# Kernel optimization log

Hardware: AMD Instinct MI355X
Metric: run time of the kernel (lower is better)

The kernel has to match this reference:

```python
import jax, jax.numpy as jnp
import numpy as np

B, S, N, H, F, L, Lt = 2, 8, 150, 128, 40, 2, 1
EF = 2 * F + 2  # 82: src feat + dst feat + distance + bond
_rows_np, _cols_np = np.where(~np.eye(N, dtype=bool))  # fully connected, no self loops
_rows = jnp.asarray(_rows_np)
_cols = jnp.asarray(_cols_np)
E = _rows_np.shape[0]


def setup_inputs() -> dict:
    key = jax.random.key(0)
    ks = jax.random.split(key, 20)
    w = lambda k, shape: 0.1 * jax.random.normal(k, shape, dtype=jnp.float32)
    d = {}
    d['t'] = jax.random.uniform(ks[0], (B, 1), dtype=jnp.float32)
    d['x'] = jax.random.normal(ks[1], (B, S, N, 3), dtype=jnp.float32)
    d['peptide_seq'] = jax.random.randint(ks[2], (B, 15), 0, 20)
    d['atom_labels'] = jax.random.randint(ks[3], (B, N), 0, 5)
    d['amino_acid_pos'] = jax.random.randint(ks[4], (B, N), 1, 16)
    d['bond_matrix'] = (jax.random.uniform(ks[5], (B, N, N)) < 0.1).astype(jnp.float32)
    d['edge_mask'] = jnp.ones((B, N, N), jnp.float32)
    d['atom_mask'] = jnp.ones((B, N, 1), jnp.float32)
    d['restore_indices'] = jnp.tile(jnp.eye(N, dtype=jnp.float32)[None], (B, 1, 1))
    d['W_e1'] = w(ks[6], (L, EF, H)); d['b_e1'] = jnp.zeros((L, H), jnp.float32)
    d['W_e2'] = w(ks[7], (L, H, H)); d['b_e2'] = jnp.zeros((L, H), jnp.float32)
    d['W_c'] = w(ks[8], (L, H, 1)); d['b_c'] = jnp.zeros((L, 1), jnp.float32)
    d['W_h'] = w(ks[9], (L, F + H, F)); d['b_h'] = jnp.zeros((L, F), jnp.float32)
    d['w_t'] = w(ks[10], (L, 1, H)); d['w_b_t'] = jnp.zeros((L, H), jnp.float32)
    d['tW_e1'] = w(ks[11], (Lt, EF, H)); d['tb_e1'] = jnp.zeros((Lt, H), jnp.float32)
    d['tW_e2'] = w(ks[12], (Lt, H, H)); d['tb_e2'] = jnp.zeros((Lt, H), jnp.float32)
    d['tW_c'] = w(ks[13], (Lt, H, 1)); d['tb_c'] = jnp.zeros((Lt, 1), jnp.float32)
    d['tW_h'] = w(ks[14], (Lt, F + H, F)); d['tb_h'] = jnp.zeros((Lt, F), jnp.float32)
    return d


def _forward(t, x, peptide_seq, atom_labels, amino_acid_pos, bond_matrix, edge_mask,
             atom_mask, restore_indices, W_e1, b_e1, W_e2, b_e2, W_c, b_c, W_h, b_h,
             w_t, w_b_t, tW_e1, tb_e1, tW_e2, tb_e2, tW_c, tb_c, tW_h, tb_h):
    # single-atom embedding: [B, N, 40]
    aa = jnp.take_along_axis(peptide_seq, amino_acid_pos - 1, axis=1)
    emb = jnp.concatenate([
        jax.nn.one_hot(atom_labels, 5, dtype=x.dtype),
        jax.nn.one_hot(aa, 20, dtype=x.dtype),
        jax.nn.one_hot(amino_acid_pos - 1, 15, dtype=x.dtype)], axis=-1)
    h = jnp.broadcast_to(emb[:, None], (B, S, N, F))
    # restore absolute coordinates: x[b,s,i,d] = sum_j x[b,s,j,d] * R[b,i,j]
    x = jnp.einsum('bsjd,bij->bsid', x, restore_indices)
    x0 = x
    # per-edge masks/features (gathered once; identical math to full cdist + indexing)
    em_e = edge_mask.reshape(B, 1, N * N)[:, :, _rows * N + _cols][..., None]  # [B,1,E,1]
    bond_e = jnp.broadcast_to(bond_matrix[:, _rows, _cols][:, None, :, None], (B, S, E, 1))

    def layer(x, h, We1, be1, We2, be2, Wc, bc, Wh, bh, temb):
        diff = x[:, :, _rows] - x[:, :, _cols]                      # [B,S,E,3]
        dist = jnp.sqrt(jnp.sum(diff * diff, -1, keepdims=True) + 1e-12)
        ef = jnp.concatenate([h[:, :, _rows], h[:, :, _cols], dist, bond_e], -1)  # [B,S,E,82]
        m = jax.nn.silu(ef @ We1 + be1 + temb)
        m = jax.nn.silu(m @ We2 + be2) * em_e                        # [B,S,E,H]
        cw = m @ Wc + bc                                             # [B,S,E,1]
        x_out = jnp.zeros_like(x).at[:, :, _rows].add(diff * cw) / (N - 1)
        agg = jnp.zeros((B, S, N, m.shape[-1]), m.dtype).at[:, :, _rows].add(m)
        h_out = jax.nn.silu(jnp.concatenate([h, agg], -1) @ Wh + bh)
        return x_out, h_out

    for l in range(L):
        temb = (t @ w_t[l] + w_b_t[l])[:, None, None, :]             # [B,1,1,H]
        xo, h = layer(x, h, W_e1[l], b_e1[l], W_e2[l], b_e2[l], W_c[l], b_c[l], W_h[l], b_h[l], temb)
        x = x + xo
    for l in range(Lt):
        xo, h = layer(x, h, tW_e1[l], tb_e1[l], tW_e2[l], tb_e2[l], tW_c[l], tb_c[l], tW_h[l], tb_h[l], 0.0)
        x = x + xo
    return (x - x0) * atom_mask[:, None, :, :]


def reference(t, x, peptide_seq, atom_labels, amino_acid_pos, bond_matrix, edge_mask,
              atom_mask, restore_indices, W_e1, b_e1, W_e2, b_e2, W_c, b_c, W_h, b_h,
              w_t, w_b_t, tW_e1, tb_e1, tW_e2, tb_e2, tW_c, tb_c, tW_h, tb_h):
    return _forward(t, x, peptide_seq, atom_labels, amino_acid_pos, bond_matrix, edge_mask,
                    atom_mask, restore_indices, W_e1, b_e1, W_e2, b_e2, W_c, b_c, W_h, b_h,
                    w_t, w_b_t, tW_e1, tb_e1, tW_e2, tb_e2, tW_c, tb_c, tW_h, tb_h)
```

## Files before the change

kernel.cpp:

```cpp
#include <hip/hip_runtime.h>
#include <math.h>

#define B_ 2
#define S_ 8
#define N_ 150
#define H_ 128
#define F_ 40
#define EF_ 82
#define NP_ 160
#define MPQ 136

typedef __attribute__((ext_vector_type(8))) short short8;
typedef __attribute__((ext_vector_type(4))) float float4v;

__device__ __forceinline__ float silu_f(float v) {
    return v * __builtin_amdgcn_rcpf(1.0f + __expf(-v));
}

__device__ __forceinline__ unsigned short f2bf(float f) {
    unsigned u = __builtin_bit_cast(unsigned, f);
    return (unsigned short)((u + 0x7fffu + ((u >> 16) & 1u)) >> 16);
}

__global__ void pack_we2_kernel(const float* __restrict__ w0,
                                const float* __restrict__ w1,
                                const float* __restrict__ w2,
                                unsigned short* __restrict__ outp) {
    int e = blockIdx.x * blockDim.x + threadIdx.x;
    int l = e >> 14, idx = e & 16383;
    int k = idx >> 7, c = idx & 127;
    const float* src = (l == 0) ? w0 : (l == 1) ? w1 : w2;
    outp[l * 16384 + c * H_ + k] = f2bf(src[idx]);
}

__global__ void restore_x_kernel(const float* __restrict__ x,
                                 const float* __restrict__ R,
                                 float* __restrict__ xa,
                                 float* __restrict__ x0) {
    int idx = blockIdx.x * blockDim.x + threadIdx.x;
    if (idx >= B_ * S_ * N_ * 3) return;
    int d = idx % 3;
    int i = (idx / 3) % N_;
    int bs = idx / (3 * N_);
    int b = bs / S_;
    const float* xrow = x + bs * N_ * 3 + d;
    const float* Rrow = R + (b * N_ + i) * N_;
    float acc = 0.0f;
    for (int j = 0; j < N_; j++) acc += xrow[j * 3] * Rrow[j];
    xa[idx] = acc;
    x0[idx] = acc;
}

__global__ void node0_kernel(const int* __restrict__ pep,
                             const int* __restrict__ labels,
                             const int* __restrict__ aapos,
                             const float* __restrict__ We1,
                             const float* __restrict__ be1,
                             const float* __restrict__ tp,
                             const float* __restrict__ wt,
                             const float* __restrict__ wbt,
                             float* __restrict__ h0,
                             float* __restrict__ Af,
                             float* __restrict__ Bf) {
    int bi = blockIdx.x;
    int b = bi / N_, i = bi % N_;
    int c = threadIdx.x;
    int al = labels[bi];
    int ap = aapos[bi];
    int aa = pep[b * 15 + ap - 1];
    int r0 = al, r1 = 5 + aa, r2 = 25 + ap - 1;
    float fa = We1[r0 * H_ + c] + We1[r1 * H_ + c] + We1[r2 * H_ + c]
             + be1[c] + tp[b] * wt[c] + wbt[c];
    float fb = We1[(F_ + r0) * H_ + c] + We1[(F_ + r1) * H_ + c] + We1[(F_ + r2) * H_ + c];
    float hv = 0.0f;
    if (c < F_) hv = (c == r0 || c == r1 || c == r2) ? 1.0f : 0.0f;
    for (int s = 0; s < S_; s++) {
        int n = (b * S_ + s) * N_ + i;
        Af[n * H_ + c] = fa;
        Bf[n * H_ + c] = fb;
        if (c < F_) h0[n * F_ + c] = hv;
    }
}

__global__ void node_kernel(const float* __restrict__ h_in,
                            const float* __restrict__ agg,
                            const float* __restrict__ Wh,
                            const float* __restrict__ bh,
                            const float* __restrict__ We1n,
                            const float* __restrict__ be1n,
                            const float* __restrict__ tp,
                            const float* __restrict__ wtn,
                            const float* __restrict__ wbtn,
                            int has_t,
                            float* __restrict__ h_out,
                            float* __restrict__ Af,
                            float* __restrict__ Bf) {
    int n = blockIdx.x;
    int b = n / (S_ * N_);
    int tid = threadIdx.x;
    __shared__ float cat[F_ + H_];
    __shared__ float part[120];
    __shared__ float hnew[F_];
    if (tid < F_) cat[tid] = h_in[n * F_ + tid];
    cat[F_ + tid] = agg[n * H_ + tid];
    __syncthreads();
    if (tid < 120) {
        int f = tid % 40, ks = tid / 40;
        float p = 0.0f;
        int k0 = ks * 56;
#pragma unroll 8
        for (int k = k0; k < k0 + 56; k++) p += cat[k] * Wh[k * F_ + f];
        part[tid] = p;
    }
    __syncthreads();
    if (tid < F_) {
        float hv = silu_f(part[tid] + part[40 + tid] + part[80 + tid] + bh[tid]);
        hnew[tid] = hv;
        h_out[n * F_ + tid] = hv;
    }
    __syncthreads();
    float fa = be1n[tid] + (has_t ? tp[b] * wtn[tid] + wbtn[tid] : 0.0f);
    float fb = 0.0f;
#pragma unroll 8
    for (int k = 0; k < F_; k++) {
        float hv = hnew[k];
        fa += hv * We1n[k * H_ + tid];
        fb += hv * We1n[(F_ + k) * H_ + tid];
    }
    Af[n * H_ + tid] = fa;
    Bf[n * H_ + tid] = fb;
}

__global__ __launch_bounds__(256, 4) void edge_kernel(
    const float* __restrict__ x_in,
    const float* __restrict__ Afeat,
    const float* __restrict__ Bfeat,
    const float* __restrict__ We1,
    const unsigned short* __restrict__ we2t,
    const float* __restrict__ be2,
    const float* __restrict__ Wc,
    const float* __restrict__ bcp,
    const float* __restrict__ bond,
    const float* __restrict__ emask,
    const float* __restrict__ x0v,
    const float* __restrict__ amask,
    int final_mode,
    float* __restrict__ x_out,
    float* __restrict__ agg_out)
{
    __shared__ __align__(16) short mbuf[2][16 * MPQ];
    __shared__ float4 diffE[NP_];
    __shared__ float2 dbL[NP_];
    __shared__ float DsumL[3];
    __shared__ float wpart[4][3];

    int blk = blockIdx.x;
    int i = blk % N_, bs = blk / N_, b = bs / S_;
    int tid = threadIdx.x;
    int node = bs * N_ + i;
    int lane = tid & 63, w = tid >> 6;
    int qd = lane >> 4, l15 = lane & 15;
    int rowLoc = tid >> 4, c0 = (tid & 15) * 8;

    float xi0 = x_in[node * 3 + 0];
    float xi1 = x_in[node * 3 + 1];
    float xi2 = x_in[node * 3 + 2];

    if (tid < NP_) {
        int j = tid;
        float xj0 = xi0, xj1 = xi1, xj2 = xi2, bnd = 0.0f, emv = 0.0f;
        if (j < N_) {
            int nj = bs * N_ + j;
            xj0 = x_in[nj * 3 + 0];
            xj1 = x_in[nj * 3 + 1];
            xj2 = x_in[nj * 3 + 2];
            int eij = (b * N_ + i) * N_ + j;
            bnd = bond[eij];
            emv = (j == i) ? 0.0f : emask[eij];
        }
        float d0 = xi0 - xj0, d1 = xi1 - xj1, d2 = xi2 - xj2;
        diffE[j] = make_float4(d0, d1, d2, emv);
        dbL[j] = make_float2(sqrtf(d0 * d0 + d1 * d1 + d2 * d2 + 1e-12f), bnd);
    }

    float afr[8], w80r[8], w81r[8];
    {
        float4 t0 = *(const float4*)&Afeat[node * H_ + c0];
        float4 t1 = *(const float4*)&Afeat[node * H_ + c0 + 4];
        afr[0]=t0.x; afr[1]=t0.y; afr[2]=t0.z; afr[3]=t0.w;
        afr[4]=t1.x; afr[5]=t1.y; afr[6]=t1.z; afr[7]=t1.w;
        t0 = *(const float4*)&We1[80 * H_ + c0];
        t1 = *(const float4*)&We1[80 * H_ + c0 + 4];
        w80r[0]=t0.x; w80r[1]=t0.y; w80r[2]=t0.z; w80r[3]=t0.w;
        w80r[4]=t1.x; w80r[5]=t1.y; w80r[6]=t1.z; w80r[7]=t1.w;
        t0 = *(const float4*)&We1[81 * H_ + c0];
        t1 = *(const float4*)&We1[81 * H_ + c0 + 4];
        w81r[0]=t0.x; w81r[1]=t0.y; w81r[2]=t0.z; w81r[3]=t0.w;
        w81r[4]=t1.x; w81r[5]=t1.y; w81r[6]=t1.z; w81r[7]=t1.w;
    }

    int ctb = w * 2;
    float b2r0 = be2[ctb * 16 + l15],  b2r1 = be2[ctb * 16 + 16 + l15];
    float wc0  = Wc[ctb * 16 + l15],   wc1  = Wc[ctb * 16 + 16 + l15];
    const unsigned short* bb0 = we2t + (ctb * 16 + l15) * H_ + qd * 8;
    const unsigned short* bb1 = bb0 + 16 * H_;
    short8 bf00 = *(const short8*)(bb0 +  0);
    short8 bf01 = *(const short8*)(bb0 + 32);
    short8 bf02 = *(const short8*)(bb0 + 64);
    short8 bf03 = *(const short8*)(bb0 + 96);
    short8 bf10 = *(const short8*)(bb1 +  0);
    short8 bf11 = *(const short8*)(bb1 + 32);
    short8 bf12 = *(const short8*)(bb1 + 64);
    short8 bf13 = *(const short8*)(bb1 + 96);

    __syncthreads();

    if (w == 0) {
        float p0 = 0, p1 = 0, p2 = 0;
        for (int j = lane; j < NP_; j += 64) {
            float4 d = diffE[j];
            p0 += d.x; p1 += d.y; p2 += d.z;
        }
        for (int s = 1; s < 64; s <<= 1) {
            p0 += __shfl_xor(p0, s, 64);
            p1 += __shfl_xor(p1, s, 64);
            p2 += __shfl_xor(p2, s, 64);
        }
        if (lane == 0) { DsumL[0] = p0; DsumL[1] = p1; DsumL[2] = p2; }
    }

    float aggP0 = 0, aggP1 = 0;
    float SP00 = 0, SP01 = 0, SP02 = 0, SP10 = 0, SP11 = 0, SP12 = 0;

    for (int jt = 0; jt < 10; jt++) {
        short* mb = mbuf[jt & 1];
        int jrow = jt * 16 + rowLoc;
        float mv[8];
        if (jrow < N_) {
            const float* bp = &Bfeat[(bs * N_ + jrow) * H_ + c0];
            float4 b0 = *(const float4*)bp;
            float4 b1 = *(const float4*)(bp + 4);
            float br[8] = {b0.x, b0.y, b0.z, b0.w, b1.x, b1.y, b1.z, b1.w};
            float2 db = dbL[jrow];
#pragma unroll
            for (int u = 0; u < 8; u++)
                mv[u] = silu_f(afr[u] + br[u] + db.x * w80r[u] + db.y * w81r[u]);
        } else {
#pragma unroll
            for (int u = 0; u < 8; u++) mv[u] = 0.0f;
        }
        short8 pkv;
#pragma unroll
        for (int u = 0; u < 8; u++) pkv[u] = (short)f2bf(mv[u]);
        *(short8*)&mb[rowLoc * MPQ + c0] = pkv;
        __syncthreads();

        const short* arow = &mb[l15 * MPQ + qd * 8];
        short8 a0 = *(const short8*)(arow +  0);
        short8 a1 = *(const short8*)(arow + 32);
        short8 a2 = *(const short8*)(arow + 64);
        short8 a3 = *(const short8*)(arow + 96);
        float4v acc0 = {0, 0, 0, 0}, acc1 = {0, 0, 0, 0};
        acc0 = __builtin_amdgcn_mfma_f32_16x16x32_bf16(a0, bf00, acc0, 0, 0, 0);
        acc1 = __builtin_amdgcn_mfma_f32_16x16x32_bf16(a0, bf10, acc1, 0, 0, 0);
        acc0 = __builtin_amdgcn_mfma_f32_16x16x32_bf16(a1, bf01, acc0, 0, 0, 0);
        acc1 = __builtin_amdgcn_mfma_f32_16x16x32_bf16(a1, bf11, acc1, 0, 0, 0);
        acc0 = __builtin_amdgcn_mfma_f32_16x16x32_bf16(a2, bf02, acc0, 0, 0, 0);
        acc1 = __builtin_amdgcn_mfma_f32_16x16x32_bf16(a2, bf12, acc1, 0, 0, 0);
        acc0 = __builtin_amdgcn_mfma_f32_16x16x32_bf16(a3, bf03, acc0, 0, 0, 0);
        acc1 = __builtin_amdgcn_mfma_f32_16x16x32_bf16(a3, bf13, acc1, 0, 0, 0);

#pragma unroll
        for (int r = 0; r < 4; r++) {
            int j = jt * 16 + qd * 4 + r;
            float4 de = diffE[j];
            float mv0 = silu_f(acc0[r] + b2r0) * de.w;
            float mv1 = silu_f(acc1[r] + b2r1) * de.w;
            aggP0 += mv0; aggP1 += mv1;
            SP00 += de.x * mv0; SP01 += de.y * mv0; SP02 += de.z * mv0;
            SP10 += de.x * mv1; SP11 += de.y * mv1; SP12 += de.z * mv1;
        }
    }

#define QR_(v) { v += __shfl_xor(v, 16, 64); v += __shfl_xor(v, 32, 64); }
    QR_(aggP0) QR_(aggP1)
    QR_(SP00) QR_(SP01) QR_(SP02)
    QR_(SP10) QR_(SP11) QR_(SP12)
#undef QR_

    if (!final_mode && qd == 0) {
        agg_out[node * H_ + ctb * 16 + l15]      = aggP0;
        agg_out[node * H_ + ctb * 16 + 16 + l15] = aggP1;
    }

    float p0 = wc0 * SP00 + wc1 * SP10;
    float p1 = wc0 * SP01 + wc1 * SP11;
    float p2 = wc0 * SP02 + wc1 * SP12;
    for (int s = 1; s < 16; s <<= 1) {
        p0 += __shfl_xor(p0, s, 64);
        p1 += __shfl_xor(p1, s, 64);
        p2 += __shfl_xor(p2, s, 64);
    }
    if (lane == 0) { wpart[w][0] = p0; wpart[w][1] = p1; wpart[w][2] = p2; }
    __syncthreads();
    if (tid < 3) {
        float tot = wpart[0][tid] + wpart[1][tid] + wpart[2][tid] + wpart[3][tid]
                  + bcp[0] * DsumL[tid];
        float xn = x_in[node * 3 + tid] + tot * (1.0f / (float)(N_ - 1));
        if (final_mode)
            x_out[node * 3 + tid] = (xn - x0v[node * 3 + tid]) * amask[b * N_ + i];
        else
            x_out[node * 3 + tid] = xn;
    }
}

extern "C" void kernel_launch(void* const* d_in, const int* in_sizes, int n_in,
                              void* d_out, int out_size, void* d_ws, size_t ws_size,
                              hipStream_t stream) {
    const float* t     = (const float*)d_in[0];
    const float* x     = (const float*)d_in[1];
    const int*   pep   = (const int*)d_in[2];
    const int*   labels= (const int*)d_in[3];
    const int*   aapos = (const int*)d_in[4];
    const float* bond  = (const float*)d_in[5];
    const float* em    = (const float*)d_in[6];
    const float* amask = (const float*)d_in[7];
    const float* R     = (const float*)d_in[8];
    const float* W_e1  = (const float*)d_in[9];
    const float* b_e1  = (const float*)d_in[10];
    const float* W_e2  = (const float*)d_in[11];
    const float* b_e2  = (const float*)d_in[12];
    const float* W_c   = (const float*)d_in[13];
    const float* b_c   = (const float*)d_in[14];
    const float* W_h   = (const float*)d_in[15];
    const float* b_h   = (const float*)d_in[16];
    const float* w_t   = (const float*)d_in[17];
    const float* w_b_t = (const float*)d_in[18];
    const float* tW_e1 = (const float*)d_in[19];
    const float* tb_e1 = (const float*)d_in[20];
    const float* tW_e2 = (const float*)d_in[21];
    const float* tb_e2 = (const float*)d_in[22];
    const float* tW_c  = (const float*)d_in[23];
    const float* tb_c  = (const float*)d_in[24];
    float* out = (float*)d_out;

    float* ws = (float*)d_ws;
    unsigned short* we2t = (unsigned short*)ws;
    float* x0  = ws + 24576;
    float* xA  = x0 + 7200;
    float* xB  = xA + 7200;
    float* hA  = xB + 7200;
    float* hB  = hA + 96000;
    float* agg = hB + 96000;
    float* Af  = agg + 307200;
    float* Bf  = Af + 307200;

    const int XE = B_ * S_ * N_ * 3;
    const int NB = B_ * S_ * N_;

    pack_we2_kernel<<<48, 1024, 0, stream>>>(W_e2, W_e2 + H_ * H_, tW_e2, we2t);
    restore_x_kernel<<<(XE + 255) / 256, 256, 0, stream>>>(x, R, xA, x0);
    node0_kernel<<<B_ * N_, H_, 0, stream>>>(pep, labels, aapos, W_e1, b_e1,
                                             t, w_t, w_b_t, hA, Af, Bf);

    edge_kernel<<<NB, 256, 0, stream>>>(xA, Af, Bf, W_e1, we2t, b_e2, W_c, b_c,
                                        bond, em, nullptr, nullptr, 0, xB, agg);
    node_kernel<<<NB, H_, 0, stream>>>(hA, agg, W_h, b_h,
                                       W_e1 + EF_ * H_, b_e1 + H_,
                                       t, w_t + H_, w_b_t + H_, 1, hB, Af, Bf);

    edge_kernel<<<NB, 256, 0, stream>>>(xB, Af, Bf, W_e1 + EF_ * H_, we2t + 16384,
                                        b_e2 + H_, W_c + H_, b_c + 1,
                                        bond, em, nullptr, nullptr, 0, xA, agg);
    node_kernel<<<NB, H_, 0, stream>>>(hB, agg, W_h + (F_ + H_) * F_, b_h + F_,
                                       tW_e1, tb_e1,
                                       nullptr, nullptr, nullptr, 0, hA, Af, Bf);

    edge_kernel<<<NB, 256, 0, stream>>>(xA, Af, Bf, tW_e1, we2t + 32768,
                                        tb_e2, tW_c, tb_c,
                                        bond, em, x0, amask, 1, out, agg);
}
```

Baseline: 280.2 us.

## Fuse node update into edge kernel and merge prelude kernels

The per-node MLP that updates h and computes the next layer's A/B edge features now runs at the end of the edge kernel. It consumes the aggregated messages straight from shared memory, so the agg buffer round trip and two node-kernel launches go away. The three setup kernels (weight packing, coordinate restore, initial embedding) are merged into one launch with branch-by-block-index. Af/Bf are double-buffered so a layer never overwrites features that other blocks are still reading. In exchange, the edge kernel's tail adds extra shared memory and serial work on a subset of threads, which could reduce occupancy.

```diff
diff --git a/kernel.cpp b/kernel.cpp
--- a/kernel.cpp
+++ b/kernel.cpp
@@ -22,116 +22,71 @@
     return (unsigned short)((u + 0x7fffu + ((u >> 16) & 1u)) >> 16);
 }
 
-__global__ void pack_we2_kernel(const float* __restrict__ w0,
-                                const float* __restrict__ w1,
-                                const float* __restrict__ w2,
-                                unsigned short* __restrict__ outp) {
-    int e = blockIdx.x * blockDim.x + threadIdx.x;
-    int l = e >> 14, idx = e & 16383;
-    int k = idx >> 7, c = idx & 127;
-    const float* src = (l == 0) ? w0 : (l == 1) ? w1 : w2;
-    outp[l * 16384 + c * H_ + k] = f2bf(src[idx]);
-}
-
-__global__ void restore_x_kernel(const float* __restrict__ x,
-                                 const float* __restrict__ R,
-                                 float* __restrict__ xa,
-                                 float* __restrict__ x0) {
-    int idx = blockIdx.x * blockDim.x + threadIdx.x;
-    if (idx >= B_ * S_ * N_ * 3) return;
-    int d = idx % 3;
-    int i = (idx / 3) % N_;
-    int bs = idx / (3 * N_);
-    int b = bs / S_;
-    const float* xrow = x + bs * N_ * 3 + d;
-    const float* Rrow = R + (b * N_ + i) * N_;
-    float acc = 0.0f;
-    for (int j = 0; j < N_; j++) acc += xrow[j * 3] * Rrow[j];
-    xa[idx] = acc;
-    x0[idx] = acc;
-}
-
-__global__ void node0_kernel(const int* __restrict__ pep,
-                             const int* __restrict__ labels,
-                             const int* __restrict__ aapos,
-                             const float* __restrict__ We1,
-                             const float* __restrict__ be1,
-                             const float* __restrict__ tp,
-                             const float* __restrict__ wt,
-                             const float* __restrict__ wbt,
-                             float* __restrict__ h0,
-                             float* __restrict__ Af,
-                             float* __restrict__ Bf) {
-    int bi = blockIdx.x;
-    int b = bi / N_, i = bi % N_;
-    int c = threadIdx.x;
-    int al = labels[bi];
-    int ap = aapos[bi];
-    int aa = pep[b * 15 + ap - 1];
-    int r0 = al, r1 = 5 + aa, r2 = 25 + ap - 1;
-    float fa = We1[r0 * H_ + c] + We1[r1 * H_ + c] + We1[r2 * H_ + c]
-             + be1[c] + tp[b] * wt[c] + wbt[c];
-    float fb = We1[(F_ + r0) * H_ + c] + We1[(F_ + r1) * H_ + c] + We1[(F_ + r2) * H_ + c];
-    float hv = 0.0f;
-    if (c < F_) hv = (c == r0 || c == r1 || c == r2) ? 1.0f : 0.0f;
-    for (int s = 0; s < S_; s++) {
-        int n = (b * S_ + s) * N_ + i;
-        Af[n * H_ + c] = fa;
-        Bf[n * H_ + c] = fb;
-        if (c < F_) h0[n * F_ + c] = hv;
-    }
-}
-
-__global__ void node_kernel(const float* __restrict__ h_in,
-                            const float* __restrict__ agg,
-                            const float* __restrict__ Wh,
-                            const float* __restrict__ bh,
-                            const float* __restrict__ We1n,
-                            const float* __restrict__ be1n,
-                            const float* __restrict__ tp,
-                            const float* __restrict__ wtn,
-                            const float* __restrict__ wbtn,
-                            int has_t,
-                            float* __restrict__ h_out,
-                            float* __restrict__ Af,
-                            float* __restrict__ Bf) {
-    int n = blockIdx.x;
-    int b = n / (S_ * N_);
+__global__ void prelude_kernel(const float* __restrict__ w0,
+                               const float* __restrict__ w1,
+                               const float* __restrict__ w2,
+                               unsigned short* __restrict__ we2t,
+                               const float* __restrict__ x,
+                               const float* __restrict__ R,
+                               float* __restrict__ xa,
+                               float* __restrict__ x0,
+                               const int* __restrict__ pep,
+                               const int* __restrict__ labels,
+                               const int* __restrict__ aapos,
+                               const float* __restrict__ We1,
+                               const float* __restrict__ be1,
+                               const float* __restrict__ tp,
+                               const float* __restrict__ wt,
+                               const float* __restrict__ wbt,
+                               float* __restrict__ h0,
+                               float* __restrict__ Af,
+                               float* __restrict__ Bf) {
+    int bid = blockIdx.x;
     int tid = threadIdx.x;
-    __shared__ float cat[F_ + H_];
-    __shared__ float part[120];
-    __shared__ float hnew[F_];
-    if (tid < F_) cat[tid] = h_in[n * F_ + tid];
-    cat[F_ + tid] = agg[n * H_ + tid];
-    __syncthreads();
-    if (tid < 120) {
-        int f = tid % 40, ks = tid / 40;
-        float p = 0.0f;
-        int k0 = ks * 56;
-#pragma unroll 8
-        for (int k = k0; k < k0 + 56; k++) p += cat[k] * Wh[k * F_ + f];
-        part[tid] = p;
-    }
-    __syncthreads();
-    if (tid < F_) {
-        float hv = silu_f(part[tid] + part[40 + tid] + part[80 + tid] + bh[tid]);
-        hnew[tid] = hv;
-        h_out[n * F_ + tid] = hv;
-    }
-    __syncthreads();
-    float fa = be1n[tid] + (has_t ? tp[b] * wtn[tid] + wbtn[tid] : 0.0f);
-    float fb = 0.0f;
-#pragma unroll 8
-    for (int k = 0; k < F_; k++) {
-        float hv = hnew[k];
-        fa += hv * We1n[k * H_ + tid];
-        fb += hv * We1n[(F_ + k) * H_ + tid];
-    }
-    Af[n * H_ + tid] = fa;
-    Bf[n * H_ + tid] = fb;
-}
-
-__global__ __launch_bounds__(256, 4) void edge_kernel(
+    if (bid < 192) {
+        int e = bid * 256 + tid;
+        int l = e >> 14, idx = e & 16383;
+        int k = idx >> 7, c = idx & 127;
+        const float* src = (l == 0) ? w0 : (l == 1) ? w1 : w2;
+        we2t[l * 16384 + c * H_ + k] = f2bf(src[idx]);
+    } else if (bid < 221) {
+        int idx = (bid - 192) * 256 + tid;
+        if (idx < B_ * S_ * N_ * 3) {
+            int d = idx % 3;
+            int i = (idx / 3) % N_;
+            int bs = idx / (3 * N_);
+            int b = bs / S_;
+            const float* xrow = x + bs * N_ * 3 + d;
+            const float* Rrow = R + (b * N_ + i) * N_;
+            float acc = 0.0f;
+            for (int j = 0; j < N_; j++) acc += xrow[j * 3] * Rrow[j];
+            xa[idx] = acc;
+            x0[idx] = acc;
+        }
+    } else {
+        int rel = bid - 221;
+        int bi = rel * 2 + (tid >> 7);
+        int b = bi / N_, i = bi % N_;
+        int c = tid & 127;
+        int al = labels[bi];
+        int ap = aapos[bi];
+        int aa = pep[b * 15 + ap - 1];
+        int r0 = al, r1 = 5 + aa, r2 = 25 + ap - 1;
+        float fa = We1[r0 * H_ + c] + We1[r1 * H_ + c] + We1[r2 * H_ + c]
+                 + be1[c] + tp[b] * wt[c] + wbt[c];
+        float fb = We1[(F_ + r0) * H_ + c] + We1[(F_ + r1) * H_ + c] + We1[(F_ + r2) * H_ + c];
+        float hv = 0.0f;
+        if (c < F_) hv = (c == r0 || c == r1 || c == r2) ? 1.0f : 0.0f;
+        for (int s = 0; s < S_; s++) {
+            int n = (b * S_ + s) * N_ + i;
+            Af[n * H_ + c] = fa;
+            Bf[n * H_ + c] = fb;
+            if (c < F_) h0[n * F_ + c] = hv;
+        }
+    }
+}
+
+__global__ __launch_bounds__(256, 4) void edge_fused_kernel(
     const float* __restrict__ x_in,
     const float* __restrict__ Afeat,
     const float* __restrict__ Bfeat,
@@ -142,17 +97,31 @@
     const float* __restrict__ bcp,
     const float* __restrict__ bond,
     const float* __restrict__ emask,
+    const float* __restrict__ h_in,
+    const float* __restrict__ Wh,
+    const float* __restrict__ bh,
+    const float* __restrict__ We1n,
+    const float* __restrict__ be1n,
+    const float* __restrict__ tp,
+    const float* __restrict__ wtn,
+    const float* __restrict__ wbtn,
+    int has_t,
     const float* __restrict__ x0v,
     const float* __restrict__ amask,
     int final_mode,
     float* __restrict__ x_out,
-    float* __restrict__ agg_out)
+    float* __restrict__ h_out,
+    float* __restrict__ Af_out,
+    float* __restrict__ Bf_out)
 {
     __shared__ __align__(16) short mbuf[2][16 * MPQ];
     __shared__ float4 diffE[NP_];
     __shared__ float2 dbL[NP_];
     __shared__ float DsumL[3];
     __shared__ float wpart[4][3];
+    __shared__ float catL[F_ + H_];
+    __shared__ float partL[120];
+    __shared__ float hnewL[F_];
 
     int blk = blockIdx.x;
     int i = blk % N_, bs = blk / N_, b = bs / S_;
@@ -288,9 +257,12 @@
     QR_(SP10) QR_(SP11) QR_(SP12)
 #undef QR_
 
-    if (!final_mode && qd == 0) {
-        agg_out[node * H_ + ctb * 16 + l15]      = aggP0;
-        agg_out[node * H_ + ctb * 16 + 16 + l15] = aggP1;
+    if (!final_mode) {
+        if (qd == 0) {
+            catL[F_ + ctb * 16 + l15]      = aggP0;
+            catL[F_ + ctb * 16 + 16 + l15] = aggP1;
+        }
+        if (tid < F_) catL[tid] = h_in[node * F_ + tid];
     }
 
     float p0 = wc0 * SP00 + wc1 * SP10;
@@ -311,6 +283,36 @@
             x_out[node * 3 + tid] = (xn - x0v[node * 3 + tid]) * amask[b * N_ + i];
         else
             x_out[node * 3 + tid] = xn;
+    }
+
+    if (final_mode) return;
+
+    if (tid < 120) {
+        int f = tid % 40, ks = tid / 40;
+        float p = 0.0f;
+        int k0 = ks * 56;
+#pragma unroll 8
+        for (int k = k0; k < k0 + 56; k++) p += catL[k] * Wh[k * F_ + f];
+        partL[tid] = p;
+    }
+    __syncthreads();
+    if (tid < F_) {
+        float hv = silu_f(partL[tid] + partL[40 + tid] + partL[80 + tid] + bh[tid]);
+        hnewL[tid] = hv;
+        h_out[node * F_ + tid] = hv;
+    }
+    __syncthreads();
+    if (tid < H_) {
+        float fa = be1n[tid] + (has_t ? tp[b] * wtn[tid] + wbtn[tid] : 0.0f);
+        float fb = 0.0f;
+#pragma unroll 8
+        for (int k = 0; k < F_; k++) {
+            float hv = hnewL[k];
+            fa += hv * We1n[k * H_ + tid];
+            fb += hv * We1n[(F_ + k) * H_ + tid];
+        }
+        Af_out[node * H_ + tid] = fa;
+        Bf_out[node * H_ + tid] = fb;
     }
 }
 
@@ -351,32 +353,34 @@
     float* xB  = xA + 7200;
     float* hA  = xB + 7200;
     float* hB  = hA + 96000;
-    float* agg = hB + 96000;
-    float* Af  = agg + 307200;
-    float* Bf  = Af + 307200;
-
-    const int XE = B_ * S_ * N_ * 3;
+    float* Af1 = hB + 96000;
+    float* Bf1 = Af1 + 307200;
+    float* Af2 = Bf1 + 307200;
+    float* Bf2 = Af2 + 307200;
+
     const int NB = B_ * S_ * N_;
 
-    pack_we2_kernel<<<48, 1024, 0, stream>>>(W_e2, W_e2 + H_ * H_, tW_e2, we2t);
-    restore_x_kernel<<<(XE + 255) / 256, 256, 0, stream>>>(x, R, xA, x0);
-    node0_kernel<<<B_ * N_, H_, 0, stream>>>(pep, labels, aapos, W_e1, b_e1,
-                                             t, w_t, w_b_t, hA, Af, Bf);
-
-    edge_kernel<<<NB, 256, 0, stream>>>(xA, Af, Bf, W_e1, we2t, b_e2, W_c, b_c,
-                                        bond, em, nullptr, nullptr, 0, xB, agg);
-    node_kernel<<<NB, H_, 0, stream>>>(hA, agg, W_h, b_h,
-                                       W_e1 + EF_ * H_, b_e1 + H_,
-                                       t, w_t + H_, w_b_t + H_, 1, hB, Af, Bf);
-
-    edge_kernel<<<NB, 256, 0, stream>>>(xB, Af, Bf, W_e1 + EF_ * H_, we2t + 16384,
-                                        b_e2 + H_, W_c + H_, b_c + 1,
-                                        bond, em, nullptr, nullptr, 0, xA, agg);
-    node_kernel<<<NB, H_, 0, stream>>>(hB, agg, W_h + (F_ + H_) * F_, b_h + F_,
-                                       tW_e1, tb_e1,
-                                       nullptr, nullptr, nullptr, 0, hA, Af, Bf);
-
-    edge_kernel<<<NB, 256, 0, stream>>>(xA, Af, Bf, tW_e1, we2t + 32768,
-                                        tb_e2, tW_c, tb_c,
-                                        bond, em, x0, amask, 1, out, agg);
-}
+    prelude_kernel<<<371, 256, 0, stream>>>(W_e2, W_e2 + H_ * H_, tW_e2, we2t,
+                                            x, R, xA, x0,
+                                            pep, labels, aapos, W_e1, b_e1,
+                                            t, w_t, w_b_t, hA, Af1, Bf1);
+
+    edge_fused_kernel<<<NB, 256, 0, stream>>>(
+        xA, Af1, Bf1, W_e1, we2t, b_e2, W_c, b_c, bond, em,
+        hA, W_h, b_h, W_e1 + EF_ * H_, b_e1 + H_, t, w_t + H_, w_b_t + H_, 1,
+        nullptr, nullptr, 0,
+        xB, hB, Af2, Bf2);
+
+    edge_fused_kernel<<<NB, 256, 0, stream>>>(
+        xB, Af2, Bf2, W_e1 + EF_ * H_, we2t + 16384, b_e2 + H_, W_c + H_, b_c + 1,
+        bond, em,
+        hB, W_h + (F_ + H_) * F_, b_h + F_, tW_e1, tb_e1, nullptr, nullptr, nullptr, 0,
+        nullptr, nullptr, 0,
+        xA, hA, Af1, Bf1);
+
+    edge_fused_kernel<<<NB, 256, 0, stream>>>(
+        xA, Af1, Bf1, tW_e1, we2t + 32768, tb_e2, tW_c, tb_c, bond, em,
+        nullptr, nullptr, nullptr, nullptr, nullptr, nullptr, nullptr, nullptr, 0,
+        x0, amask, 1,
+        out, nullptr, nullptr, nullptr);
+}
```

Measured after the change: 269.9 us. 1.04x faster.
